# Kernel optimization log

Hardware: AMD Instinct MI355X
Metric: run time of the kernel (lower is better)

The kernel has to match this reference:

```python
import jax, jax.numpy as jnp
import numpy as np

B, H, W = 4, 1024, 1024

# 8-tap Sobel-style stencil: offsets in (u, v) units of (dx, dy)
OFF_U = jnp.array([-1.0, -1.0, -1.0, 0.0, 0.0, 1.0, 1.0, 1.0], dtype=jnp.float32)
OFF_V = jnp.array([-1.0, 0.0, 1.0, -1.0, 1.0, -1.0, 0.0, 1.0], dtype=jnp.float32)
KU = jnp.array([-0.25, -0.5, -0.25, 0.0, 0.0, 0.25, 0.5, 0.25], dtype=jnp.float32)
KV = jnp.array([-0.25, 0.0, 0.25, -0.5, 0.5, -0.25, 0.0, 0.25], dtype=jnp.float32)


def setup_inputs() -> dict:
    key = jax.random.key(0)
    k1, k2 = jax.random.split(key)
    x = jax.random.uniform(k1, (B, 3, H, W), dtype=jnp.float32)
    sigma = jax.random.uniform(k2, (B,), dtype=jnp.float32) * 2.0 + 0.5  # pixels
    return {"x": x, "sigma": sigma}


def _bilinear(tex, u, v):
    # tex: [3, H, W]; u, v: [8, H, W] normalized UV in [0,1]
    Hh, Ww = tex.shape[1], tex.shape[2]
    px = u * Ww - 0.5
    py = v * Hh - 0.5
    x0 = jnp.floor(px)
    y0 = jnp.floor(py)
    fx = (px - x0)[None]  # [1,8,H,W]
    fy = (py - y0)[None]
    x0i = jnp.clip(x0.astype(jnp.int32), 0, Ww - 1)
    x1i = jnp.clip(x0i + 1, 0, Ww - 1)
    y0i = jnp.clip(y0.astype(jnp.int32), 0, Hh - 1)
    y1i = jnp.clip(y0i + 1, 0, Hh - 1)
    t00 = tex[:, y0i, x0i]  # [3,8,H,W]
    t01 = tex[:, y0i, x1i]
    t10 = tex[:, y1i, x0i]
    t11 = tex[:, y1i, x1i]
    return (t00 * (1 - fx) * (1 - fy) + t01 * fx * (1 - fy)
            + t10 * (1 - fx) * fy + t11 * fx * fy)


def reference(x, sigma):
    Bb, C, Hh, Ww = x.shape
    ys, xs = jnp.meshgrid(jnp.arange(Hh, dtype=x.dtype),
                          jnp.arange(Ww, dtype=x.dtype), indexing='ij')
    u0 = (xs + 0.5) / Ww  # pixel-center UV
    v0 = (ys + 0.5) / Hh
    dx = sigma / Ww  # [B]
    dy = sigma / Hh
    u = u0[None, None] + OFF_U[None, :, None, None] * dx[:, None, None, None]  # [B,8,H,W]
    v = v0[None, None] + OFF_V[None, :, None, None] * dy[:, None, None, None]
    s = jax.vmap(_bilinear)(x, u, v)  # [B,3,8,H,W]
    s_u = jnp.einsum('bcthw,t->bchw', s, KU)
    s_v = jnp.einsum('bcthw,t->bchw', s, KV)
    lum = jnp.array([100.0, 1.0, 1.0], dtype=x.dtype)[None, :, None, None]
    s_u = s_u * lum
    s_v = s_v * lum
    # structure tensor components E, G, F
    return jnp.stack([(s_u * s_u).sum(1), (s_v * s_v).sum(1), (s_u * s_v).sum(1)], axis=1)
```

## Files before the change

### kernel.cpp

```cpp
#include <hip/hip_runtime.h>


#define W_ 1024
#define H_ 1024

__device__ __forceinline__ float lerp1(float a, float b, float f) {
    return fmaf(f, b - a, a);
}

__global__ __launch_bounds__(256) void st_kernel(
    const float* __restrict__ X, const float* __restrict__ S,
    float* __restrict__ O)
{
    int idx = blockIdx.x * 256 + threadIdx.x;
    int b   = idx >> 20;
    int rem = idx & 0xFFFFF;
    int y   = rem >> 10;
    int xi  = rem & 1023;

    float sg = S[b];
    float imf = floorf(-sg), ipf = floorf(sg);
    float fm  = -sg - imf;
    float fp  =  sg - ipf;
    int   im  = (int)imf, ip = (int)ipf;

    int cm0 = min(max(xi + im, 0), W_ - 1), cm1 = min(cm0 + 1, W_ - 1);
    int cp0 = min(max(xi + ip, 0), W_ - 1), cp1 = min(cp0 + 1, W_ - 1);
    int rm0 = min(max(y + im, 0), H_ - 1),  rm1 = min(rm0 + 1, H_ - 1);
    int rp0 = min(max(y + ip, 0), H_ - 1),  rp1 = min(rp0 + 1, H_ - 1);

    int o_rm0 = rm0 << 10, o_rm1 = rm1 << 10;
    int o_rp0 = rp0 << 10, o_rp1 = rp1 << 10;
    int o_r0  = y   << 10;

    float oxx = 0.f, oyy = 0.f, oxy = 0.f;

    #pragma unroll
    for (int c = 0; c < 3; ++c) {
        const float* base = X + (((size_t)(b * 3 + c)) << 20);

        float hm_m0 = lerp1(base[o_rm0 + cm0], base[o_rm0 + cm1], fm);
        float hm_m1 = lerp1(base[o_rm1 + cm0], base[o_rm1 + cm1], fm);
        float hm_0  = lerp1(base[o_r0  + cm0], base[o_r0  + cm1], fm);
        float hm_p0 = lerp1(base[o_rp0 + cm0], base[o_rp0 + cm1], fm);
        float hm_p1 = lerp1(base[o_rp1 + cm0], base[o_rp1 + cm1], fm);
        float hp_m0 = lerp1(base[o_rm0 + cp0], base[o_rm0 + cp1], fp);
        float hp_m1 = lerp1(base[o_rm1 + cp0], base[o_rm1 + cp1], fp);
        float hp_0  = lerp1(base[o_r0  + cp0], base[o_r0  + cp1], fp);
        float hp_p0 = lerp1(base[o_rp0 + cp0], base[o_rp0 + cp1], fp);
        float hp_p1 = lerp1(base[o_rp1 + cp0], base[o_rp1 + cp1], fp);
        float h0_m0 = base[o_rm0 + xi], h0_m1 = base[o_rm1 + xi];
        float h0_p0 = base[o_rp0 + xi], h0_p1 = base[o_rp1 + xi];

        float t0 = lerp1(hm_m0, hm_m1, fm);
        float t1 = hm_0;
        float t2 = lerp1(hm_p0, hm_p1, fp);
        float t3 = lerp1(h0_m0, h0_m1, fm);
        float t4 = lerp1(h0_p0, h0_p1, fp);
        float t5 = lerp1(hp_m0, hp_m1, fm);
        float t6 = hp_0;
        float t7 = lerp1(hp_p0, hp_p1, fp);

        float su = 0.25f * (t5 + t7 - t0 - t2) + 0.5f * (t6 - t1);
        float sv = 0.25f * (t2 + t7 - t0 - t5) + 0.5f * (t4 - t3);

        float l2 = (c == 0) ? 10000.f : 1.f;
        oxx = fmaf(l2 * su, su, oxx);
        oyy = fmaf(l2 * sv, sv, oyy);
        oxy = fmaf(l2 * su, sv, oxy);
    }

    size_t obase = ((size_t)(b * 3)) << 20;
    int pix = (y << 10) | xi;
    O[obase + pix]             = oxx;
    O[obase + (1 << 20) + pix] = oyy;
    O[obase + (2 << 20) + pix] = oxy;
}

extern "C" void kernel_launch(void* const* d_in, const int* in_sizes, int n_in,
                              void* d_out, int out_size, void* d_ws, size_t ws_size,
                              hipStream_t stream) {
    const float* x     = (const float*)d_in[0];
    const float* sigma = (const float*)d_in[1];
    float* out = (float*)d_out;

    dim3 grid(4 * 1024 * 1024 / 256), block(256);
    hipLaunchKernelGGL(st_kernel, grid, block, 0, stream, x, sigma, out);
}
```

Before: 130.0 us.

## Compute 8 vertical pixels per thread with sliding-row reuse of horizontal lerps

Each thread now produces an 8-pixel column strip. Every input row is loaded and horizontally interpolated once, then its contribution is scattered into the outputs it affects through precomputed vertical coefficients, specialised per integer sigma offset via templates. This is meant to remove the redundant row loads and lerps that neighbouring pixels repeat in the per-pixel version. In exchange, register use rises. Border tiles and non-integer-compatible sigmas fall back to a slower per-pixel path, and the threads of a block may diverge between the two paths.

```diff
diff --git a/kernel.cpp b/kernel.cpp
--- a/kernel.cpp
+++ b/kernel.cpp
@@ -3,22 +3,15 @@
 
 #define W_ 1024
 #define H_ 1024
+#define PLANE (1 << 20)
 
 __device__ __forceinline__ float lerp1(float a, float b, float f) {
     return fmaf(f, b - a, a);
 }
 
-__global__ __launch_bounds__(256) void st_kernel(
-    const float* __restrict__ X, const float* __restrict__ S,
-    float* __restrict__ O)
+__device__ void slow_pixel(const float* __restrict__ Xb, float* __restrict__ Ob,
+                           float sg, int xi, int y)
 {
-    int idx = blockIdx.x * 256 + threadIdx.x;
-    int b   = idx >> 20;
-    int rem = idx & 0xFFFFF;
-    int y   = rem >> 10;
-    int xi  = rem & 1023;
-
-    float sg = S[b];
     float imf = floorf(-sg), ipf = floorf(sg);
     float fm  = -sg - imf;
     float fp  =  sg - ipf;
@@ -37,7 +30,7 @@
 
     #pragma unroll
     for (int c = 0; c < 3; ++c) {
-        const float* base = X + (((size_t)(b * 3 + c)) << 20);
+        const float* base = Xb + ((size_t)c << 20);
 
         float hm_m0 = lerp1(base[o_rm0 + cm0], base[o_rm0 + cm1], fm);
         float hm_m1 = lerp1(base[o_rm1 + cm0], base[o_rm1 + cm1], fm);
@@ -70,11 +63,113 @@
         oxy = fmaf(l2 * su, sv, oxy);
     }
 
-    size_t obase = ((size_t)(b * 3)) << 20;
     int pix = (y << 10) | xi;
-    O[obase + pix]             = oxx;
-    O[obase + (1 << 20) + pix] = oyy;
-    O[obase + (2 << 20) + pix] = oxy;
+    Ob[pix]             = oxx;
+    Ob[PLANE + pix]     = oyy;
+    Ob[2 * PLANE + pix] = oxy;
+}
+
+template<int IP>
+__device__ void fast8(const float* __restrict__ Xb, float* __restrict__ Ob,
+                      float sg, int x, int y0)
+{
+    constexpr int D  = 2 * IP + 3;
+    constexpr int RW = 10 + 2 * IP;
+
+    float fp = sg - (float)IP;
+    float fm = 1.0f - fp;
+
+    float cu[D], cv[D], cw[D];
+    #pragma unroll
+    for (int j = 0; j < D; ++j) { cu[j] = 0.f; cv[j] = 0.f; cw[j] = 0.f; }
+    cu[0]        += 0.25f * fp; cv[0]        -= 0.25f * fp; cw[0]        -= 0.5f * fp;
+    cu[1]        += 0.25f * fm; cv[1]        -= 0.25f * fm; cw[1]        -= 0.5f * fm;
+    cu[IP + 1]   += 0.5f;
+    cu[2*IP + 1] += 0.25f * fm; cv[2*IP + 1] += 0.25f * fm; cw[2*IP + 1] += 0.5f * fm;
+    cu[2*IP + 2] += 0.25f * fp; cv[2*IP + 2] += 0.25f * fp; cw[2*IP + 2] += 0.5f * fp;
+
+    int cm0 = max(x - (IP + 1), 0);
+    int cm1 = cm0 + 1;
+    int cp0 = min(x + IP, W_ - 1);
+    int cp1 = min(cp0 + 1, W_ - 1);
+
+    float oxx[8], oyy[8], oxy[8];
+    #pragma unroll
+    for (int k = 0; k < 8; ++k) { oxx[k] = 0.f; oyy[k] = 0.f; oxy[k] = 0.f; }
+
+    #pragma unroll
+    for (int c = 0; c < 3; ++c) {
+        const float* base = Xb + ((size_t)c << 20) + ((y0 - IP - 1) << 10);
+        float su[8], sv[8];
+        #pragma unroll
+        for (int k = 0; k < 8; ++k) { su[k] = 0.f; sv[k] = 0.f; }
+
+        #pragma unroll
+        for (int w = 0; w < RW; ++w) {
+            const float* rp = base + (w << 10);
+            float a0 = rp[cm0], a1 = rp[cm1];
+            float b0 = rp[cp0], b1 = rp[cp1];
+            float cc = rp[x];
+            float hm = lerp1(a0, a1, fm);
+            float hp = lerp1(b0, b1, fp);
+            float q = hp - hm;
+            float s = hm + hp;
+            #pragma unroll
+            for (int j = 0; j < D; ++j) {
+                int k = w - j;
+                if (k >= 0 && k < 8) {
+                    su[k] = fmaf(cu[j], q, su[k]);
+                    sv[k] = fmaf(cv[j], s, sv[k]);
+                    sv[k] = fmaf(cw[j], cc, sv[k]);
+                }
+            }
+        }
+
+        float l2 = (c == 0) ? 10000.f : 1.f;
+        #pragma unroll
+        for (int k = 0; k < 8; ++k) {
+            oxx[k] = fmaf(l2 * su[k], su[k], oxx[k]);
+            oyy[k] = fmaf(l2 * sv[k], sv[k], oyy[k]);
+            oxy[k] = fmaf(l2 * su[k], sv[k], oxy[k]);
+        }
+    }
+
+    #pragma unroll
+    for (int k = 0; k < 8; ++k) {
+        int pix = ((y0 + k) << 10) | x;
+        Ob[pix]             = oxx[k];
+        Ob[PLANE + pix]     = oyy[k];
+        Ob[2 * PLANE + pix] = oxy[k];
+    }
+}
+
+__global__ __launch_bounds__(256, 4) void st_kernel(
+    const float* __restrict__ X, const float* __restrict__ S,
+    float* __restrict__ O)
+{
+    int x  = blockIdx.x * 256 + threadIdx.x;
+    int y0 = blockIdx.y * 8;
+    int b  = blockIdx.z;
+
+    const float* Xb = X + (size_t)b * 3 * PLANE;
+    float*       Ob = O + (size_t)b * 3 * PLANE;
+    float sg = S[b];
+
+    int ip = (int)floorf(sg);
+    int im = (int)floorf(-sg);
+    bool sig_ok = (im == -ip - 1) && ip >= 0 && ip <= 2;
+    bool fast   = sig_ok && (y0 - ip - 1 >= 0) && (y0 + 8 + ip <= H_ - 1);
+
+    if (fast) {
+        switch (ip) {
+            case 0:  fast8<0>(Xb, Ob, sg, x, y0); break;
+            case 1:  fast8<1>(Xb, Ob, sg, x, y0); break;
+            default: fast8<2>(Xb, Ob, sg, x, y0); break;
+        }
+    } else {
+        for (int k = 0; k < 8; ++k)
+            slow_pixel(Xb, Ob, sg, x, y0 + k);
+    }
 }
 
 extern "C" void kernel_launch(void* const* d_in, const int* in_sizes, int n_in,
@@ -84,6 +179,6 @@
     const float* sigma = (const float*)d_in[1];
     float* out = (float*)d_out;
 
-    dim3 grid(4 * 1024 * 1024 / 256), block(256);
+    dim3 grid(W_ / 256, H_ / 8, 4), block(256);
     hipLaunchKernelGGL(st_kernel, grid, block, 0, stream, x, sigma, out);
 }
```

Measured after the change: 165.8 us. 27.6% more time.

## Compute 4x2 pixel tiles per thread with separable row-sweep and vector loads

Applied to the files above, without the earlier changes.

Replaces the one-pixel-per-thread stencil with a register-tiled path in which each thread computes a 4x2 output block. It sweeps the needed input rows once with float4 loads, accumulates the bilinear-stencil contributions row by row, and specializes on the integer part of sigma through templates. Border columns and rows, and unusual sigma values, fall back to the original per-pixel routine via an extra block row and a runtime check. This is meant to cut redundant global loads and index math, at the cost of more registers, heavier code and branch divergence at the edges.

```diff
diff --git a/kernel.cpp b/kernel.cpp
--- a/kernel.cpp
+++ b/kernel.cpp
@@ -3,22 +3,15 @@
 
 #define W_ 1024
 #define H_ 1024
+#define PLANE (1 << 20)
 
 __device__ __forceinline__ float lerp1(float a, float b, float f) {
     return fmaf(f, b - a, a);
 }
 
-__global__ __launch_bounds__(256) void st_kernel(
-    const float* __restrict__ X, const float* __restrict__ S,
-    float* __restrict__ O)
+__device__ void slow_pixel(const float* __restrict__ Xb, float* __restrict__ Ob,
+                           float sg, int xi, int y)
 {
-    int idx = blockIdx.x * 256 + threadIdx.x;
-    int b   = idx >> 20;
-    int rem = idx & 0xFFFFF;
-    int y   = rem >> 10;
-    int xi  = rem & 1023;
-
-    float sg = S[b];
     float imf = floorf(-sg), ipf = floorf(sg);
     float fm  = -sg - imf;
     float fp  =  sg - ipf;
@@ -37,7 +30,7 @@
 
     #pragma unroll
     for (int c = 0; c < 3; ++c) {
-        const float* base = X + (((size_t)(b * 3 + c)) << 20);
+        const float* base = Xb + ((size_t)c << 20);
 
         float hm_m0 = lerp1(base[o_rm0 + cm0], base[o_rm0 + cm1], fm);
         float hm_m1 = lerp1(base[o_rm1 + cm0], base[o_rm1 + cm1], fm);
@@ -70,11 +63,168 @@
         oxy = fmaf(l2 * su, sv, oxy);
     }
 
-    size_t obase = ((size_t)(b * 3)) << 20;
     int pix = (y << 10) | xi;
-    O[obase + pix]             = oxx;
-    O[obase + (1 << 20) + pix] = oyy;
-    O[obase + (2 << 20) + pix] = oxy;
+    Ob[pix]             = oxx;
+    Ob[PLANE + pix]     = oyy;
+    Ob[2 * PLANE + pix] = oxy;
+}
+
+template<int N>
+__device__ __forceinline__ void acc(float (&arr)[N], int k, float val) {
+    if (k >= 0 && k < N) arr[k] += val;
+}
+
+template<int IP>
+__device__ void fast42(const float* __restrict__ Xb, float* __restrict__ Ob,
+                       float fp, float fm, int x0, int y0)
+{
+    constexpr int RW = 2 + 2 * IP + 2;
+    constexpr int EA = 3 - IP;
+    constexpr int EB = 4 + IP;
+
+    int g0 = max(x0 - 4, 0);
+    int g1 = x0;
+    int g2 = min(x0 + 4, W_ - 4);
+
+    float oxx[4][2], oyy[4][2], oxy[4][2];
+    #pragma unroll
+    for (int j = 0; j < 4; ++j)
+        #pragma unroll
+        for (int k = 0; k < 2; ++k) {
+            oxx[j][k] = 0.f; oyy[j][k] = 0.f; oxy[j][k] = 0.f;
+        }
+
+    #pragma unroll
+    for (int c = 0; c < 3; ++c) {
+        const float* rowp = Xb + ((size_t)c << 20) + ((y0 - IP - 1) << 10);
+        float su[4][2], sv[4][2];
+        #pragma unroll
+        for (int j = 0; j < 4; ++j) {
+            su[j][0] = 0.f; su[j][1] = 0.f;
+            sv[j][0] = 0.f; sv[j][1] = 0.f;
+        }
+
+        #pragma unroll
+        for (int w = 0; w < RW; ++w) {
+            const float* rp = rowp + (w << 10);
+            float4 A4 = *reinterpret_cast<const float4*>(rp + g0);
+            float4 B4 = *reinterpret_cast<const float4*>(rp + g1);
+            float4 C4 = *reinterpret_cast<const float4*>(rp + g2);
+            float wv[12] = {A4.x, A4.y, A4.z, A4.w,
+                            B4.x, B4.y, B4.z, B4.w,
+                            C4.x, C4.y, C4.z, C4.w};
+
+            #pragma unroll
+            for (int j = 0; j < 4; ++j) {
+                float hm = lerp1(wv[j + EA], wv[j + EA + 1], fm);
+                float hp = lerp1(wv[j + EB], wv[j + EB + 1], fp);
+                float cc = wv[j + 4];
+                float q  = hp - hm;
+                float A  = 0.25f * q;
+                float hq = 0.5f  * q;
+                float Bv = fmaf(0.25f, hm + hp, 0.5f * cc);
+                float fpA = fp * A,  fmA = fm * A;
+                float fpB = fp * Bv, fmB = fm * Bv;
+
+                acc(su[j], w,              fpA);
+                acc(su[j], w - 1,          fmA);
+                acc(su[j], w - IP - 1,     hq);
+                acc(su[j], w - 2*IP - 1,   fmA);
+                acc(su[j], w - 2*IP - 2,   fpA);
+                acc(sv[j], w,             -fpB);
+                acc(sv[j], w - 1,         -fmB);
+                acc(sv[j], w - 2*IP - 1,   fmB);
+                acc(sv[j], w - 2*IP - 2,   fpB);
+            }
+        }
+
+        float l2 = (c == 0) ? 10000.f : 1.f;
+        #pragma unroll
+        for (int j = 0; j < 4; ++j)
+            #pragma unroll
+            for (int k = 0; k < 2; ++k) {
+                oxx[j][k] = fmaf(l2 * su[j][k], su[j][k], oxx[j][k]);
+                oyy[j][k] = fmaf(l2 * sv[j][k], sv[j][k], oyy[j][k]);
+                oxy[j][k] = fmaf(l2 * su[j][k], sv[j][k], oxy[j][k]);
+            }
+    }
+
+    bool ok[4];
+    #pragma unroll
+    for (int j = 0; j < 4; ++j)
+        ok[j] = (x0 + j > IP) && (x0 + j < W_ - 1 - IP);
+    bool all4 = ok[0] && ok[1] && ok[2] && ok[3];
+
+    #pragma unroll
+    for (int k = 0; k < 2; ++k) {
+        int pix = ((y0 + k) << 10) | x0;
+        if (all4) {
+            *reinterpret_cast<float4*>(Ob + pix) =
+                make_float4(oxx[0][k], oxx[1][k], oxx[2][k], oxx[3][k]);
+            *reinterpret_cast<float4*>(Ob + PLANE + pix) =
+                make_float4(oyy[0][k], oyy[1][k], oyy[2][k], oyy[3][k]);
+            *reinterpret_cast<float4*>(Ob + 2 * PLANE + pix) =
+                make_float4(oxy[0][k], oxy[1][k], oxy[2][k], oxy[3][k]);
+        } else {
+            #pragma unroll
+            for (int j = 0; j < 4; ++j) {
+                if (ok[j]) {
+                    Ob[pix + j]             = oxx[j][k];
+                    Ob[PLANE + pix + j]     = oyy[j][k];
+                    Ob[2 * PLANE + pix + j] = oxy[j][k];
+                }
+            }
+        }
+    }
+}
+
+__global__ __launch_bounds__(256) void st_kernel(
+    const float* __restrict__ X, const float* __restrict__ S,
+    float* __restrict__ O)
+{
+    int b  = blockIdx.z;
+    const float* Xb = X + (size_t)b * 3 * PLANE;
+    float*       Ob = O + (size_t)b * 3 * PLANE;
+    float sg = S[b];
+
+    if (blockIdx.y == (H_ / 8)) {
+        int tid = blockIdx.x * 256 + threadIdx.y * 64 + threadIdx.x;
+        #pragma unroll
+        for (int it = 0; it < 6; ++it) {
+            int pidx = tid + it * 1024;
+            if (pidx < 6144) {
+                int yy = pidx / 6;
+                int cc = pidx - yy * 6;
+                int xx = (cc < 3) ? cc : (W_ - 6 + cc);
+                slow_pixel(Xb, Ob, sg, xx, yy);
+            }
+        }
+        return;
+    }
+
+    int x0 = (blockIdx.x * 64 + threadIdx.x) * 4;
+    int y0 = blockIdx.y * 8 + threadIdx.y * 2;
+
+    int ipv = (int)floorf(sg);
+    int imv = (int)floorf(-sg);
+    bool sig_ok = (imv == -ipv - 1) && ipv >= 0 && ipv <= 2;
+    bool rows_ok = (y0 >= ipv + 1) && (y0 <= H_ - 3 - ipv);
+    float fp = sg - (float)ipv;
+    float fm = 1.0f - fp;
+
+    if (sig_ok && rows_ok) {
+        switch (ipv) {
+            case 0:  fast42<0>(Xb, Ob, fp, fm, x0, y0); break;
+            case 1:  fast42<1>(Xb, Ob, fp, fm, x0, y0); break;
+            default: fast42<2>(Xb, Ob, fp, fm, x0, y0); break;
+        }
+    } else {
+        #pragma unroll
+        for (int k = 0; k < 2; ++k)
+            #pragma unroll
+            for (int j = 0; j < 4; ++j)
+                slow_pixel(Xb, Ob, sg, x0 + j, y0 + k);
+    }
 }
 
 extern "C" void kernel_launch(void* const* d_in, const int* in_sizes, int n_in,
@@ -84,6 +234,6 @@
     const float* sigma = (const float*)d_in[1];
     float* out = (float*)d_out;
 
-    dim3 grid(4 * 1024 * 1024 / 256), block(256);
+    dim3 grid(4, H_ / 8 + 1, 4), block(64, 4);
     hipLaunchKernelGGL(st_kernel, grid, block, 0, stream, x, sigma, out);
 }
```

Result: slower. 146.4 us (+12.6%).
